# Performance work log

Measured on AMD Instinct MI355X. Metric: run time of the kernel, lower is better.

The kernel has to match this reference:

```python
import jax, jax.numpy as jnp
import numpy as np

B, N, D = 4, 2048, 1024
HEAD_DIMS = 128
NUM_HEADS = 8
PROJ = HEAD_DIMS * NUM_HEADS  # 1024


def setup_inputs() -> dict:
    key = jax.random.key(0)
    ks = jax.random.split(key, 5)
    # Weights stored as (in, out); xavier-normal-like scale
    def xavier(k, fan_in, fan_out):
        std = (2.0 / (fan_in + fan_out)) ** 0.5
        return jax.random.normal(k, (fan_in, fan_out), dtype=jnp.float32) * std
    return {
        "x": jax.random.normal(ks[0], (B, N, D), dtype=jnp.float32),
        "Wq": xavier(ks[1], D, PROJ),
        "Wk": xavier(ks[2], D, PROJ),
        "Wv": xavier(ks[3], D, PROJ),
        "Wo": xavier(ks[4], PROJ, PROJ),
    }


def reference(x, Wq, Wk, Wv, Wo):
    b, n, d = x.shape
    # QKV projections, split into heads: (b, h, n, hd)
    def split_heads(z):
        return z.reshape(b, n, NUM_HEADS, HEAD_DIMS).transpose(0, 2, 1, 3)
    q = split_heads(x @ Wq)
    k = split_heads(x @ Wk)
    v = split_heads(x @ Wv)
    scale = 1.0 / jnp.sqrt(jnp.float32(HEAD_DIMS))
    logits = jnp.einsum("bhqd,bhkd->bhqk", q, k) * scale
    weights = jax.nn.softmax(logits, axis=-1)
    out = jnp.einsum("bhqk,bhkd->bhqd", weights, v)
    out = out.transpose(0, 2, 1, 3).reshape(b, n, PROJ)
    return out @ Wo
```

## Files before the change

kernel.cpp:

```cpp
#include <hip/hip_runtime.h>
#include <hip/hip_bf16.h>


typedef __attribute__((ext_vector_type(8))) short short8;
typedef __attribute__((ext_vector_type(4))) short short4v;
typedef __attribute__((ext_vector_type(4))) float floatx4;
typedef __attribute__((ext_vector_type(8))) _Float16 half8;

#define MFMA_F16(a, b, c) __builtin_amdgcn_mfma_f32_16x16x32_f16( \
    __builtin_bit_cast(half8, (a)), __builtin_bit_cast(half8, (b)), (c), 0, 0, 0)

static constexpr int BATCH  = 4;
static constexpr int NHEADS = 8;
static constexpr int SEQ    = 2048;
static constexpr int HD     = 128;
static constexpr int DMODEL = 1024;
static constexpr int MROWS  = BATCH * SEQ;
static constexpr int NQKV   = 3 * DMODEL;

#define QSCALE2 0.12752283786512624f

static __device__ __forceinline__ short f16bits(float v) {
    return __builtin_bit_cast(short, (_Float16)v);
}

template <typename T>
static __device__ __forceinline__ short8 load8_f16(const T* p) {
    if constexpr (sizeof(T) == 2) {
        return *(const short8*)p;
    } else {
        const float4 f0 = *(const float4*)p;
        const float4 f1 = *(const float4*)(p + 4);
        short8 r;
        r[0] = f16bits(f0.x); r[1] = f16bits(f0.y);
        r[2] = f16bits(f0.z); r[3] = f16bits(f0.w);
        r[4] = f16bits(f1.x); r[5] = f16bits(f1.y);
        r[6] = f16bits(f1.z); r[7] = f16bits(f1.w);
        return r;
    }
}

static __device__ __forceinline__ void storeC(float* C, size_t idx, float v) {
    C[idx] = v;
}
static __device__ __forceinline__ void storeC(_Float16* C, size_t idx, float v) {
    C[idx] = (_Float16)v;
}

static __device__ __forceinline__ void gload16(const short* g, short* l) {
    __builtin_amdgcn_global_load_lds(
        (const __attribute__((address_space(1))) void*)g,
        (__attribute__((address_space(3))) void*)l, 16, 0, 0);
}

__global__ __launch_bounds__(256)
void prep(const float* __restrict__ x, short* __restrict__ xb,
          const float* __restrict__ W0, const float* __restrict__ W1,
          const float* __restrict__ W2, const float* __restrict__ W3,
          short* __restrict__ Wt, int K, int N)
{
    __shared__ short T[32][33];
    const int z = blockIdx.z;
    if (z >= 4) {
        const size_t chunk = ((size_t)(z - 4) * 1024 + blockIdx.y * 32 + blockIdx.x);
        const size_t i = (chunk * 256 + threadIdx.x) * 8;
        *(short8*)&xb[i] = load8_f16(&x[i]);
        return;
    }
    const float* W = (z == 0) ? W0 : (z == 1) ? W1 : (z == 2) ? W2 : W3;
    short* Wtz = Wt + (size_t)z * K * N;

    const int n0 = blockIdx.x * 32, k0 = blockIdx.y * 32;
    const int r = threadIdx.x >> 3, c4 = (threadIdx.x & 7) * 4;

    const float4 v = *(const float4*)&W[(size_t)(k0 + r) * N + n0 + c4];
    T[r][c4 + 0] = f16bits(v.x);
    T[r][c4 + 1] = f16bits(v.y);
    T[r][c4 + 2] = f16bits(v.z);
    T[r][c4 + 3] = f16bits(v.w);
    __syncthreads();

    short4v o;
    o[0] = T[c4 + 0][r]; o[1] = T[c4 + 1][r];
    o[2] = T[c4 + 2][r]; o[3] = T[c4 + 3][r];
    *(short4v*)&Wtz[(size_t)(n0 + r) * K + k0 + c4] = o;
}

__global__ __launch_bounds__(256)
void convx(const float* __restrict__ x, short* __restrict__ xb)
{
    const size_t i = ((size_t)blockIdx.x * 256 + threadIdx.x) * 8;
    *(short8*)&xb[i] = load8_f16(&x[i]);
}

__global__ __launch_bounds__(256)
void transpose_v(const short* __restrict__ V, short* __restrict__ Vt)
{
    __shared__ short T[64][72];
    const int s0 = blockIdx.x * 64;
    const int d0 = blockIdx.y * 64;
    const int bh = blockIdx.z;
    const short* Vi = V  + (size_t)bh * SEQ * HD;
    short*       Vo = Vt + (size_t)bh * HD * SEQ;

    const int r = threadIdx.x >> 3;
    const int c = threadIdx.x & 7;

    *(short8*)&T[r][c * 8]      = *(const short8*)&Vi[(size_t)(s0 + r) * HD + d0 + c * 8];
    *(short8*)&T[r + 32][c * 8] = *(const short8*)&Vi[(size_t)(s0 + r + 32) * HD + d0 + c * 8];
    __syncthreads();

    short8 o0, o1;
    #pragma unroll
    for (int j = 0; j < 8; ++j) {
        o0[j] = T[c * 8 + j][r];
        o1[j] = T[c * 8 + j][r + 32];
    }
    *(short8*)&Vo[(size_t)(d0 + r) * SEQ + s0 + c * 8]      = o0;
    *(short8*)&Vo[(size_t)(d0 + r + 32) * SEQ + s0 + c * 8] = o1;
}

template <typename OutT, bool QKV>
__global__ __launch_bounds__(256)
void gemm128(const short* __restrict__ A, const short* __restrict__ Bt,
             OutT* __restrict__ C, int M, int N, int K, size_t qkvStride)
{
    __shared__ __align__(16) short As[128 * 64];
    __shared__ __align__(16) short Bs[128 * 64];

    const int tid  = threadIdx.x;
    const int lane = tid & 63;
    const int w    = tid >> 6;
    const int quad = lane >> 4;
    const int l16  = lane & 15;

    const int m0 = blockIdx.x * 128;
    const int n0 = blockIdx.y * 128;
    const int wm = (w >> 1) * 64;
    const int wn = (w & 1) * 64;

    floatx4 acc[4][4] = {};

    const int srow   = tid >> 3;
    const int schunk = (tid & 7) ^ (srow & 7);
    const short* aG = A  + (size_t)(m0 + srow) * K + schunk * 8;
    const short* bG = Bt + (size_t)(n0 + srow) * K + schunk * 8;
    short* aL = As + tid * 8;
    short* bL = Bs + tid * 8;

    const int fsw = l16 & 7;

    for (int k0 = 0; k0 < K; k0 += 64) {
        __syncthreads();
        #pragma unroll
        for (int r = 0; r < 4; ++r) {
            gload16(aG + k0 + (size_t)(r * 32) * K, aL + r * 2048);
            gload16(bG + k0 + (size_t)(r * 32) * K, bL + r * 2048);
        }
        __syncthreads();

        #pragma unroll
        for (int kk = 0; kk < 2; ++kk) {
            short8 af[4], bf[4];
            #pragma unroll
            for (int mi = 0; mi < 4; ++mi)
                af[mi] = *(short8*)&As[(wm + mi * 16 + l16) * 64 +
                                       (((kk * 4 + quad) ^ fsw) * 8)];
            #pragma unroll
            for (int ni = 0; ni < 4; ++ni)
                bf[ni] = *(short8*)&Bs[(wn + ni * 16 + l16) * 64 +
                                       (((kk * 4 + quad) ^ fsw) * 8)];

            #pragma unroll
            for (int mi = 0; mi < 4; ++mi)
                #pragma unroll
                for (int ni = 0; ni < 4; ++ni)
                    acc[mi][ni] = MFMA_F16(af[mi], bf[ni], acc[mi][ni]);
        }
    }

    #pragma unroll
    for (int mi = 0; mi < 4; ++mi)
        #pragma unroll
        for (int ni = 0; ni < 4; ++ni)
            #pragma unroll
            for (int r = 0; r < 4; ++r) {
                const int m = m0 + wm + mi * 16 + quad * 4 + r;
                const int n = n0 + wn + ni * 16 + l16;
                float v = acc[mi][ni][r];
                if constexpr (QKV) {
                    const int qkv = n >> 10, rem = n & 1023;
                    const int h = rem >> 7, d = rem & 127;
                    const int b = m >> 11, s = m & 2047;
                    if (qkv == 0) v *= QSCALE2;
                    storeC(C, (size_t)qkv * qkvStride +
                              (((size_t)b * NHEADS + h) * SEQ + s) * HD + d, v);
                } else {
                    storeC(C, (size_t)m * N + n, v);
                }
            }
}

__global__ __launch_bounds__(256)
void attn_flash10(const short* __restrict__ Q, const short* __restrict__ K,
                  const short* __restrict__ Vt, _Float16* __restrict__ O)
{
    __shared__ __align__(16) short Ks[2][32 * 128];
    __shared__ __align__(16) short Vs[2][128 * 32];
    __shared__ __align__(16) short Plds[4][16 * 40];

    const int tid  = threadIdx.x;
    const int lane = tid & 63;
    const int w    = tid >> 6;
    const int quad = lane >> 4;
    const int l16  = lane & 15;

    const int h  = blockIdx.x & 7;
    const int qi = blockIdx.x >> 3;
    const int b  = blockIdx.y;
    const int q0 = qi * 64;

    const short* Qh  = Q  + (((size_t)b * NHEADS + h) * SEQ) * HD;
    const short* Kh  = K  + (((size_t)b * NHEADS + h) * SEQ) * HD;
    const short* Vth = Vt + (((size_t)b * NHEADS + h) * HD) * SEQ;

    const int qrow = q0 + w * 16 + l16;
    short8 qf[4];
    #pragma unroll
    for (int c = 0; c < 4; ++c)
        qf[c] = *(const short8*)&Qh[(size_t)qrow * HD + c * 32 + quad * 8];

    const int kr0 = tid >> 4, kc0 = tid & 15;
    const int kr1 = kr0 + 16;
    const short* kGa = Kh + (size_t)kr0 * HD + ((kc0 ^ (kr0 & 15)) * 8);
    const short* kGb = Kh + (size_t)kr1 * HD + ((kc0 ^ (kr1 & 15)) * 8);
    const int vr0 = tid >> 2, vp0 = tid & 3;
    const short* vGa = Vth + (size_t)vr0 * SEQ + ((vp0 ^ ((vr0 >> 1) & 3)) * 8);
    const short* vGb = Vth + (size_t)(vr0 + 64) * SEQ + ((vp0 ^ ((vr0 >> 1) & 3)) * 8);

    floatx4 acc[8] = {};
    floatx4 acc9 = {};

    short8 ones;
    #pragma unroll
    for (int j = 0; j < 8; ++j) ones[j] = 0x3C00;

    const int fswV = (l16 >> 1) & 3;
    short* Pw = &Plds[w][0];

    auto STAGE = [&](short* kDst, short* vDst, int tile) {
        const size_t ko = (size_t)tile * 32 * HD;
        const size_t vo = (size_t)tile * 32;
        gload16(kGa + ko, kDst + tid * 8);
        gload16(kGb + ko, kDst + (tid + 256) * 8);
        gload16(vGa + vo, vDst + tid * 8);
        gload16(vGb + vo, vDst + (tid + 256) * 8);
    };

    auto COMPUTE = [&](const short* Kb, const short* Vb) {
        floatx4 s0 = {}, s1 = {};
        __builtin_amdgcn_s_setprio(1);
        #pragma unroll
        for (int c = 0; c < 4; ++c) {
            const int k_ = c * 4 + quad;
            short8 kf0 = *(short8*)&Kb[l16 * 128 + ((k_ ^ l16) * 8)];
            short8 kf1 = *(short8*)&Kb[(16 + l16) * 128 + ((k_ ^ l16) * 8)];
            s0 = MFMA_F16(qf[c], kf0, s0);
            s1 = MFMA_F16(qf[c], kf1, s1);
        }
        __builtin_amdgcn_s_setprio(0);
        #pragma unroll
        for (int r = 0; r < 4; ++r) {
            const float p0 = __builtin_amdgcn_exp2f(s0[r]);
            const float p1 = __builtin_amdgcn_exp2f(s1[r]);
            Pw[(quad * 4 + r) * 40 + l16]      = f16bits(p0);
            Pw[(quad * 4 + r) * 40 + 16 + l16] = f16bits(p1);
        }
        short8 pf = *(short8*)&Pw[l16 * 40 + quad * 8];
        __builtin_amdgcn_s_setprio(1);
        acc9 = MFMA_F16(pf, ones, acc9);
        #pragma unroll
        for (int hc = 0; hc < 8; ++hc) {
            short8 vf = *(short8*)&Vs[0][0];
            vf = *(short8*)&Vb[(hc * 16 + l16) * 32 + ((quad ^ fswV) * 8)];
            acc[hc] = MFMA_F16(pf, vf, acc[hc]);
        }
        __builtin_amdgcn_s_setprio(0);
    };

    STAGE(&Ks[0][0], &Vs[0][0], 0);

    for (int kt = 0; kt < SEQ; kt += 64) {
        const int t = kt >> 5;
        __syncthreads();
        STAGE(&Ks[1][0], &Vs[1][0], t + 1);
        COMPUTE(&Ks[0][0], &Vs[0][0]);
        __syncthreads();
        if (kt + 64 < SEQ)
            STAGE(&Ks[0][0], &Vs[0][0], t + 2);
        COMPUTE(&Ks[1][0], &Vs[1][0]);
    }

    float rinv[4];
    #pragma unroll
    for (int r = 0; r < 4; ++r)
        rinv[r] = 1.0f / fmaxf(acc9[r], 1e-30f);

    #pragma unroll
    for (int hc = 0; hc < 8; ++hc)
        #pragma unroll
        for (int r = 0; r < 4; ++r) {
            const int row = q0 + w * 16 + quad * 4 + r;
            O[((size_t)b * SEQ + row) * DMODEL + h * HD + hc * 16 + l16] =
                (_Float16)(acc[hc][r] * rinv[r]);
        }
}

template <typename AT, typename OutT>
__global__ __launch_bounds__(256)
void gemm64(const AT* __restrict__ A, const float* __restrict__ W,
            OutT* __restrict__ C, int M, int N, int K, int headsplit)
{
    __shared__ __align__(16) short As[64][32];
    __shared__ __align__(16) short Bs[64][32];

    const int tid  = threadIdx.x;
    const int lane = tid & 63;
    const int w    = tid >> 6;
    const int quad = lane >> 4;
    const int l16  = lane & 15;

    const int m0 = blockIdx.x * 64;
    const int n0 = blockIdx.y * 64;
    const int wm = (w >> 1) * 32;
    const int wn = (w & 1) * 32;

    floatx4 acc[2][2] = {};

    const int arow = tid >> 2, acol = (tid & 3) * 8;
    const int brow = tid >> 3, bcol = (tid & 7) * 8;

    const AT*    aptr = A + (size_t)(m0 + arow) * K + acol;
    const float* bptr = W + (size_t)brow * N + n0 + bcol;

    for (int k0 = 0; k0 < K; k0 += 32) {
        short8 av = load8_f16(aptr + k0);
        short8 bv = load8_f16(bptr + (size_t)k0 * N);
        __syncthreads();
        *(short8*)&As[arow][acol] = av;
        #pragma unroll
        for (int j = 0; j < 8; ++j)
            Bs[bcol + j][brow] = bv[j];
        __syncthreads();

        short8 af0 = *(short8*)&As[wm + l16][quad * 8];
        short8 af1 = *(short8*)&As[wm + 16 + l16][quad * 8];
        short8 bf0 = *(short8*)&Bs[wn + l16][quad * 8];
        short8 bf1 = *(short8*)&Bs[wn + 16 + l16][quad * 8];

        acc[0][0] = MFMA_F16(af0, bf0, acc[0][0]);
        acc[0][1] = MFMA_F16(af0, bf1, acc[0][1]);
        acc[1][0] = MFMA_F16(af1, bf0, acc[1][0]);
        acc[1][1] = MFMA_F16(af1, bf1, acc[1][1]);
    }

    #pragma unroll
    for (int mi = 0; mi < 2; ++mi)
        #pragma unroll
        for (int ni = 0; ni < 2; ++ni)
            #pragma unroll
            for (int r = 0; r < 4; ++r) {
                const int m = m0 + wm + mi * 16 + quad * 4 + r;
                const int n = n0 + wn + ni * 16 + l16;
                const float v = acc[mi][ni][r];
                if (headsplit) {
                    const int b = m >> 11, nn = m & 2047;
                    const int h = n >> 7,  d  = n & 127;
                    storeC(C, (((size_t)b * NHEADS + h) * SEQ + nn) * HD + d, v);
                } else {
                    storeC(C, (size_t)m * N + n, v);
                }
            }
}

__global__ __launch_bounds__(256)
void attn_flash(const short* __restrict__ Q, const short* __restrict__ K,
                const short* __restrict__ V, _Float16* __restrict__ O)
{
    __shared__ __align__(16) short Ksf[32][136];
    __shared__ __align__(16) short Vtl[HD][40];
    __shared__ __align__(16) short Pldsf[4][16][40];

    const int tid  = threadIdx.x;
    const int lane = tid & 63;
    const int w    = tid >> 6;
    const int quad = lane >> 4;
    const int l16  = lane & 15;

    const int q0 = blockIdx.x * 64;
    const int h  = blockIdx.y;
    const int b  = blockIdx.z;

    const size_t headoff = ((size_t)b * NHEADS + h) * SEQ * HD;
    const short* Qh = Q + headoff;
    const short* Kh = K + headoff;
    const short* Vh = V + headoff;

    const float scale = 0.08838834764831845f;

    const int qrow = q0 + w * 16 + l16;
    short8 qf[4];
    #pragma unroll
    for (int c = 0; c < 4; ++c)
        qf[c] = *(const short8*)&Qh[(size_t)qrow * HD + c * 32 + quad * 8];

    float mrow[4], lrow[4];
    #pragma unroll
    for (int r = 0; r < 4; ++r) { mrow[r] = -1e30f; lrow[r] = 0.f; }
    floatx4 acc[8] = {};

    const int krow = tid >> 4, kcol = (tid & 15) * 8;
    const int vkey = tid & 31;
    const int vhd  = (tid >> 5) * 16;

    for (int kt = 0; kt < SEQ; kt += 32) {
        const short* Kt = Kh + (size_t)kt * HD;
        short8 k0v = *(const short8*)(Kt + (size_t)tid * 8);
        short8 k1v = *(const short8*)(Kt + (size_t)(tid + 256) * 8);
        short8 v0 = *(const short8*)&Vh[(size_t)(kt + vkey) * HD + vhd];
        short8 v1 = *(const short8*)&Vh[(size_t)(kt + vkey) * HD + vhd + 8];

        __syncthreads();
        *(short8*)&Ksf[krow][kcol]      = k0v;
        *(short8*)&Ksf[krow + 16][kcol] = k1v;
        #pragma unroll
        for (int j = 0; j < 8; ++j) {
            Vtl[vhd + j][vkey]     = v0[j];
            Vtl[vhd + 8 + j][vkey] = v1[j];
        }
        __syncthreads();

        floatx4 s0 = {}, s1 = {};
        #pragma unroll
        for (int c = 0; c < 4; ++c) {
            short8 kf0 = *(short8*)&Ksf[l16][c * 32 + quad * 8];
            short8 kf1 = *(short8*)&Ksf[16 + l16][c * 32 + quad * 8];
            s0 = MFMA_F16(qf[c], kf0, s0);
            s1 = MFMA_F16(qf[c], kf1, s1);
        }

        float p0[4], p1[4], alpha[4];
        #pragma unroll
        for (int r = 0; r < 4; ++r) {
            const float a  = s0[r] * scale;
            const float bb = s1[r] * scale;
            float mx = fmaxf(a, bb);
            mx = fmaxf(mx, __shfl_xor(mx, 1));
            mx = fmaxf(mx, __shfl_xor(mx, 2));
            mx = fmaxf(mx, __shfl_xor(mx, 4));
            mx = fmaxf(mx, __shfl_xor(mx, 8));
            const float mnew = fmaxf(mrow[r], mx);
            alpha[r] = __expf(mrow[r] - mnew);
            mrow[r]  = mnew;
            p0[r] = __expf(a - mnew);
            p1[r] = __expf(bb - mnew);
            float rs = p0[r] + p1[r];
            rs += __shfl_xor(rs, 1);
            rs += __shfl_xor(rs, 2);
            rs += __shfl_xor(rs, 4);
            rs += __shfl_xor(rs, 8);
            lrow[r] = lrow[r] * alpha[r] + rs;
        }
        #pragma unroll
        for (int hc = 0; hc < 8; ++hc)
            #pragma unroll
            for (int r = 0; r < 4; ++r)
                acc[hc][r] *= alpha[r];

        #pragma unroll
        for (int r = 0; r < 4; ++r) {
            Pldsf[w][quad * 4 + r][l16]      = f16bits(p0[r]);
            Pldsf[w][quad * 4 + r][16 + l16] = f16bits(p1[r]);
        }
        __syncthreads();

        short8 pf = *(short8*)&Pldsf[w][l16][quad * 8];
        #pragma unroll
        for (int hc = 0; hc < 8; ++hc) {
            short8 vf = *(short8*)&Vtl[hc * 16 + l16][quad * 8];
            acc[hc] = MFMA_F16(pf, vf, acc[hc]);
        }
    }

    #pragma unroll
    for (int hc = 0; hc < 8; ++hc)
        #pragma unroll
        for (int r = 0; r < 4; ++r) {
            const int row = q0 + w * 16 + quad * 4 + r;
            const float val = acc[hc][r] / fmaxf(lrow[r], 1e-30f);
            O[((size_t)b * SEQ + row) * DMODEL + h * HD + hc * 16 + l16] =
                (_Float16)val;
        }
}

extern "C" void kernel_launch(void* const* d_in, const int* in_sizes, int n_in,
                              void* d_out, int out_size, void* d_ws, size_t ws_size,
                              hipStream_t stream)
{
    const float* x  = (const float*)d_in[0];
    const float* Wq = (const float*)d_in[1];
    const float* Wk = (const float*)d_in[2];
    const float* Wv = (const float*)d_in[3];
    const float* Wo = (const float*)d_in[4];
    float* out = (float*)d_out;

    const size_t bufElems = (size_t)MROWS * DMODEL;
    const size_t batElems = (size_t)SEQ * DMODEL;
    const size_t MiB = 1024 * 1024;
    dim3 tt(256);

    if (ws_size >= 72 * MiB) {
        short* xb    = (short*)d_ws;
        short* Qb    = xb + bufElems;
        short* Kb    = xb + 2 * bufElems;
        short* Vn    = xb + 3 * bufElems;
        short* Wtall = xb + 4 * bufElems;
        short* Wto   = Wtall + 3 * (size_t)DMODEL * DMODEL;
        short* VtG   = xb;
        short* Ab    = Vn;

        prep<<<dim3(32, 32, 8), tt, 0, stream>>>(
            x, xb, Wq, Wk, Wv, Wo, Wtall, DMODEL, DMODEL);

        gemm128<_Float16, true><<<dim3(MROWS / 128, NQKV / 128), tt, 0, stream>>>(
            xb, Wtall, (_Float16*)Qb, MROWS, NQKV, DMODEL, bufElems);

        transpose_v<<<dim3(SEQ / 64, HD / 64, BATCH * NHEADS), tt, 0, stream>>>(Vn, VtG);

        attn_flash10<<<dim3(NHEADS * (SEQ / 64), BATCH), tt, 0, stream>>>(
            Qb, Kb, VtG, (_Float16*)Ab);

        gemm128<float, false><<<dim3(MROWS / 128, DMODEL / 128), tt, 0, stream>>>(
            Ab, Wto, out, MROWS, DMODEL, DMODEL, 0);
    } else if (ws_size >= 64 * MiB) {
        short* xb    = (short*)d_ws;
        short* Qb    = xb + 2 * batElems;
        short* Kb    = Qb + 4 * batElems;
        short* Vn    = Kb + 4 * batElems;
        short* Wtall = Vn + 4 * batElems;
        short* Wto   = Wtall + 3 * (size_t)DMODEL * DMODEL;

        prep<<<dim3(32, 32, 4), tt, 0, stream>>>(
            nullptr, nullptr, Wq, Wk, Wv, Wo, Wtall, DMODEL, DMODEL);

        for (int half = 0; half < 2; ++half) {
            const size_t off = (size_t)half * 2 * batElems;
            convx<<<dim3(2048), tt, 0, stream>>>(x + off, xb);
            gemm128<_Float16, true><<<dim3(32, NQKV / 128), tt, 0, stream>>>(
                xb, Wtall, (_Float16*)(Qb + off), 2 * SEQ, NQKV, DMODEL,
                4 * batElems);
        }
        for (int half = 0; half < 2; ++half) {
            const size_t off = (size_t)half * 2 * batElems;
            transpose_v<<<dim3(SEQ / 64, HD / 64, 2 * NHEADS), tt, 0, stream>>>(
                Vn + off, xb);
            attn_flash10<<<dim3(NHEADS * (SEQ / 64), 2), tt, 0, stream>>>(
                Qb + off, Kb + off, xb, (_Float16*)(Vn + off));
        }
        gemm128<float, false><<<dim3(MROWS / 128, DMODEL / 128), tt, 0, stream>>>(
            Vn, Wto, out, MROWS, DMODEL, DMODEL, 0);
    } else if (ws_size >= 24 * MiB) {
        short* xb    = (short*)d_ws;
        short* Qb    = xb + batElems;
        short* Kb    = xb + 2 * batElems;
        short* Vb    = xb + 3 * batElems;
        short* Wtall = xb + 4 * batElems;
        short* Wto   = Wtall + 3 * (size_t)DMODEL * DMODEL;

        prep<<<dim3(32, 32, 4), tt, 0, stream>>>(
            nullptr, nullptr, Wq, Wk, Wv, Wo, Wtall, DMODEL, DMODEL);

        for (int b = 0; b < BATCH; ++b) {
            convx<<<dim3(1024), tt, 0, stream>>>(x + (size_t)b * batElems, xb);
            gemm128<_Float16, true><<<dim3(SEQ / 128, NQKV / 128), tt, 0, stream>>>(
                xb, Wtall, (_Float16*)Qb, SEQ, NQKV, DMODEL, batElems);
            transpose_v<<<dim3(SEQ / 64, HD / 64, NHEADS), tt, 0, stream>>>(Vb, xb);
            attn_flash10<<<dim3(NHEADS * (SEQ / 64), 1), tt, 0, stream>>>(
                Qb, Kb, xb, (_Float16*)Vb);
            gemm128<float, false><<<dim3(SEQ / 128, DMODEL / 128), tt, 0, stream>>>(
                Vb, Wto, out + (size_t)b * batElems, SEQ, DMODEL, DMODEL, 0);
        }
    } else {
        short* Qb = (short*)d_ws;
        short* Kb = Qb + batElems;
        short* Vb = Qb + 2 * batElems;
        short* Ab = Qb + 3 * batElems;

        dim3 gg(SEQ / 64, DMODEL / 64);
        for (int b = 0; b < BATCH; ++b) {
            const float* xb_ = x + (size_t)b * batElems;
            gemm64<float, _Float16><<<gg, tt, 0, stream>>>(
                xb_, Wq, (_Float16*)Qb, SEQ, DMODEL, DMODEL, 1);
            gemm64<float, _Float16><<<gg, tt, 0, stream>>>(
                xb_, Wk, (_Float16*)Kb, SEQ, DMODEL, DMODEL, 1);
            gemm64<float, _Float16><<<gg, tt, 0, stream>>>(
                xb_, Wv, (_Float16*)Vb, SEQ, DMODEL, DMODEL, 1);
            attn_flash<<<dim3(SEQ / 64, NHEADS, 1), tt, 0, stream>>>(
                Qb, Kb, Vb, (_Float16*)Ab);
            gemm64<short, float><<<gg, tt, 0, stream>>>(
                Ab, Wo, out + (size_t)b * batElems, SEQ, DMODEL, DMODEL, 0);
        }
    }
}
```

Baseline: 281.6 us.

## Fuse V transpose into QKV GEMM epilogue and drop transpose kernel

The QKV GEMM epilogue now writes V directly in transposed (head_dim x seq) layout using packed 4-element stores along the sequence dimension, so the separate transpose_v kernel and its extra read/write pass over V are removed from every workspace path. Workspace buffers are reassigned so attention output reuses the x buffer, and the 64MiB path interleaves the output GEMM per half. The transposed V stores are strided by SEQ per d, which may be less coalesced than the original row-major store. A dead shared-memory load in the attention inner loop is also removed.

```diff
diff --git a/kernel.cpp b/kernel.cpp
--- a/kernel.cpp
+++ b/kernel.cpp
@@ -93,33 +93,6 @@
     *(short8*)&xb[i] = load8_f16(&x[i]);
 }
 
-__global__ __launch_bounds__(256)
-void transpose_v(const short* __restrict__ V, short* __restrict__ Vt)
-{
-    __shared__ short T[64][72];
-    const int s0 = blockIdx.x * 64;
-    const int d0 = blockIdx.y * 64;
-    const int bh = blockIdx.z;
-    const short* Vi = V  + (size_t)bh * SEQ * HD;
-    short*       Vo = Vt + (size_t)bh * HD * SEQ;
-
-    const int r = threadIdx.x >> 3;
-    const int c = threadIdx.x & 7;
-
-    *(short8*)&T[r][c * 8]      = *(const short8*)&Vi[(size_t)(s0 + r) * HD + d0 + c * 8];
-    *(short8*)&T[r + 32][c * 8] = *(const short8*)&Vi[(size_t)(s0 + r + 32) * HD + d0 + c * 8];
-    __syncthreads();
-
-    short8 o0, o1;
-    #pragma unroll
-    for (int j = 0; j < 8; ++j) {
-        o0[j] = T[c * 8 + j][r];
-        o1[j] = T[c * 8 + j][r + 32];
-    }
-    *(short8*)&Vo[(size_t)(d0 + r) * SEQ + s0 + c * 8]      = o0;
-    *(short8*)&Vo[(size_t)(d0 + r + 32) * SEQ + s0 + c * 8] = o1;
-}
-
 template <typename OutT, bool QKV>
 __global__ __launch_bounds__(256)
 void gemm128(const short* __restrict__ A, const short* __restrict__ Bt,
@@ -182,23 +155,37 @@
     #pragma unroll
     for (int mi = 0; mi < 4; ++mi)
         #pragma unroll
-        for (int ni = 0; ni < 4; ++ni)
-            #pragma unroll
-            for (int r = 0; r < 4; ++r) {
-                const int m = m0 + wm + mi * 16 + quad * 4 + r;
-                const int n = n0 + wn + ni * 16 + l16;
-                float v = acc[mi][ni][r];
-                if constexpr (QKV) {
-                    const int qkv = n >> 10, rem = n & 1023;
-                    const int h = rem >> 7, d = rem & 127;
-                    const int b = m >> 11, s = m & 2047;
-                    if (qkv == 0) v *= QSCALE2;
-                    storeC(C, (size_t)qkv * qkvStride +
-                              (((size_t)b * NHEADS + h) * SEQ + s) * HD + d, v);
+        for (int ni = 0; ni < 4; ++ni) {
+            if constexpr (QKV) {
+                const int n   = n0 + wn + ni * 16 + l16;
+                const int qkv = n >> 10, rem = n & 1023;
+                const int hh  = rem >> 7, d = rem & 127;
+                const int mb  = m0 + wm + mi * 16 + quad * 4;
+                const int bb  = mb >> 11, s = mb & 2047;
+                if (qkv == 2) {
+                    short4v pk;
+                    #pragma unroll
+                    for (int r = 0; r < 4; ++r)
+                        pk[r] = f16bits(acc[mi][ni][r]);
+                    *(short4v*)&((short*)C)[2 * qkvStride +
+                        (((size_t)bb * NHEADS + hh) * HD + d) * SEQ + s] = pk;
                 } else {
-                    storeC(C, (size_t)m * N + n, v);
+                    const float sc = (qkv == 0) ? QSCALE2 : 1.0f;
+                    #pragma unroll
+                    for (int r = 0; r < 4; ++r)
+                        storeC(C, (size_t)qkv * qkvStride +
+                                  (((size_t)bb * NHEADS + hh) * SEQ + s + r) * HD + d,
+                               acc[mi][ni][r] * sc);
+                }
+            } else {
+                #pragma unroll
+                for (int r = 0; r < 4; ++r) {
+                    const int m = m0 + wm + mi * 16 + quad * 4 + r;
+                    const int n = n0 + wn + ni * 16 + l16;
+                    storeC(C, (size_t)m * N + n, acc[mi][ni][r]);
                 }
             }
+        }
 }
 
 __global__ __launch_bounds__(256)
@@ -281,8 +268,7 @@
         acc9 = MFMA_F16(pf, ones, acc9);
         #pragma unroll
         for (int hc = 0; hc < 8; ++hc) {
-            short8 vf = *(short8*)&Vs[0][0];
-            vf = *(short8*)&Vb[(hc * 16 + l16) * 32 + ((quad ^ fswV) * 8)];
+            short8 vf = *(short8*)&Vb[(hc * 16 + l16) * 32 + ((quad ^ fswV) * 8)];
             acc[hc] = MFMA_F16(pf, vf, acc[hc]);
         }
         __builtin_amdgcn_s_setprio(0);
@@ -523,11 +509,10 @@
         short* xb    = (short*)d_ws;
         short* Qb    = xb + bufElems;
         short* Kb    = xb + 2 * bufElems;
-        short* Vn    = xb + 3 * bufElems;
+        short* Vtb   = xb + 3 * bufElems;
         short* Wtall = xb + 4 * bufElems;
         short* Wto   = Wtall + 3 * (size_t)DMODEL * DMODEL;
-        short* VtG   = xb;
-        short* Ab    = Vn;
+        short* Ab    = xb;
 
         prep<<<dim3(32, 32, 8), tt, 0, stream>>>(
             x, xb, Wq, Wk, Wv, Wo, Wtall, DMODEL, DMODEL);
@@ -535,10 +520,8 @@
         gemm128<_Float16, true><<<dim3(MROWS / 128, NQKV / 128), tt, 0, stream>>>(
             xb, Wtall, (_Float16*)Qb, MROWS, NQKV, DMODEL, bufElems);
 
-        transpose_v<<<dim3(SEQ / 64, HD / 64, BATCH * NHEADS), tt, 0, stream>>>(Vn, VtG);
-
         attn_flash10<<<dim3(NHEADS * (SEQ / 64), BATCH), tt, 0, stream>>>(
-            Qb, Kb, VtG, (_Float16*)Ab);
+            Qb, Kb, Vtb, (_Float16*)Ab);
 
         gemm128<float, false><<<dim3(MROWS / 128, DMODEL / 128), tt, 0, stream>>>(
             Ab, Wto, out, MROWS, DMODEL, DMODEL, 0);
@@ -546,8 +529,8 @@
         short* xb    = (short*)d_ws;
         short* Qb    = xb + 2 * batElems;
         short* Kb    = Qb + 4 * batElems;
-        short* Vn    = Kb + 4 * batElems;
-        short* Wtall = Vn + 4 * batElems;
+        short* Vtb   = Kb + 4 * batElems;
+        short* Wtall = Vtb + 4 * batElems;
         short* Wto   = Wtall + 3 * (size_t)DMODEL * DMODEL;
 
         prep<<<dim3(32, 32, 4), tt, 0, stream>>>(
@@ -562,18 +545,16 @@
         }
         for (int half = 0; half < 2; ++half) {
             const size_t off = (size_t)half * 2 * batElems;
-            transpose_v<<<dim3(SEQ / 64, HD / 64, 2 * NHEADS), tt, 0, stream>>>(
-                Vn + off, xb);
             attn_flash10<<<dim3(NHEADS * (SEQ / 64), 2), tt, 0, stream>>>(
-                Qb + off, Kb + off, xb, (_Float16*)(Vn + off));
-        }
-        gemm128<float, false><<<dim3(MROWS / 128, DMODEL / 128), tt, 0, stream>>>(
-            Vn, Wto, out, MROWS, DMODEL, DMODEL, 0);
+                Qb + off, Kb + off, Vtb + off, (_Float16*)xb);
+            gemm128<float, false><<<dim3(32, DMODEL / 128), tt, 0, stream>>>(
+                xb, Wto, out + off, 2 * SEQ, DMODEL, DMODEL, 0);
+        }
     } else if (ws_size >= 24 * MiB) {
         short* xb    = (short*)d_ws;
         short* Qb    = xb + batElems;
         short* Kb    = xb + 2 * batElems;
-        short* Vb    = xb + 3 * batElems;
+        short* Vtb   = xb + 3 * batElems;
         short* Wtall = xb + 4 * batElems;
         short* Wto   = Wtall + 3 * (size_t)DMODEL * DMODEL;
 
@@ -584,11 +565,10 @@
             convx<<<dim3(1024), tt, 0, stream>>>(x + (size_t)b * batElems, xb);
             gemm128<_Float16, true><<<dim3(SEQ / 128, NQKV / 128), tt, 0, stream>>>(
                 xb, Wtall, (_Float16*)Qb, SEQ, NQKV, DMODEL, batElems);
-            transpose_v<<<dim3(SEQ / 64, HD / 64, NHEADS), tt, 0, stream>>>(Vb, xb);
             attn_flash10<<<dim3(NHEADS * (SEQ / 64), 1), tt, 0, stream>>>(
-                Qb, Kb, xb, (_Float16*)Vb);
+                Qb, Kb, Vtb, (_Float16*)xb);
             gemm128<float, false><<<dim3(SEQ / 128, DMODEL / 128), tt, 0, stream>>>(
-                Vb, Wto, out + (size_t)b * batElems, SEQ, DMODEL, DMODEL, 0);
+                xb, Wto, out + (size_t)b * batElems, SEQ, DMODEL, DMODEL, 0);
         }
     } else {
         short* Qb = (short*)d_ws;
```

Measured after the change: 275.6 us (median of 3 runs). 1.02x faster.
